# Kernel tuning notes

Measured on AMD Instinct MI355X. Metric: run time of the kernel, lower is better.

## Reference

```python
import jax, jax.numpy as jnp
import numpy as np

EMBED = 256
B, S = 4, 4096

def _linear_params(key, d):
    k1, k2 = jax.random.split(key)
    lim = 1.0 / np.sqrt(d)
    W = jax.random.uniform(k1, (d, d), jnp.float32, -lim, lim)
    b = jax.random.uniform(k2, (d,), jnp.float32, -lim, lim)
    return W, b

def setup_inputs() -> dict:
    key = jax.random.key(0)
    ks = jax.random.split(key, 6)
    x = jax.random.normal(ks[0], (B, S, EMBED), jnp.float32)
    Wq, bq = _linear_params(ks[1], EMBED)
    Wk, bk = _linear_params(ks[2], EMBED)
    Wv, bv = _linear_params(ks[3], EMBED)
    Wl, bl = _linear_params(ks[4], EMBED)
    g1 = jnp.ones((EMBED,), jnp.float32); be1 = jnp.zeros((EMBED,), jnp.float32)
    g2 = jnp.ones((EMBED,), jnp.float32); be2 = jnp.zeros((EMBED,), jnp.float32)
    return {"x": x, "Wq": Wq, "bq": bq, "Wk": Wk, "bk": bk, "Wv": Wv, "bv": bv,
            "Wl": Wl, "bl": bl, "g1": g1, "be1": be1, "g2": g2, "be2": be2}

def _layernorm(x, g, b, eps=1e-5):
    mu = jnp.mean(x, axis=-1, keepdims=True)
    var = jnp.mean(jnp.square(x - mu), axis=-1, keepdims=True)
    return (x - mu) * jax.lax.rsqrt(var + eps) * g + b

def reference(x, Wq, bq, Wk, bk, Wv, bv, Wl, bl, g1, be1, g2, be2):
    d = x.shape[-1]
    q = jnp.einsum('bsd,ed->bse', x, Wq) + bq
    k = jnp.einsum('bsd,ed->bse', x, Wk) + bk
    v = jnp.einsum('bsd,ed->bse', x, Wv) + bv
    scores = jnp.einsum('bqd,bkd->bqk', q, k) / np.sqrt(d).astype(np.float32)
    attn = jax.nn.softmax(scores, axis=-1)
    out = jnp.einsum('bqk,bkd->bqd', attn, v)
    h = _layernorm(x + out, g1, be1)
    # NOTE: same linear applied twice (as in the original module)
    h = jnp.einsum('bsd,ed->bse', h, Wl) + bl
    h = jax.nn.relu(h)
    h = jnp.einsum('bsd,ed->bse', h, Wl) + bl
    return _layernorm(x + h, g2, be2)
```

## Files before the change

### kernel.cpp

```cpp
#include <hip/hip_runtime.h>

typedef unsigned short u16;
typedef float  f32x4 __attribute__((ext_vector_type(4)));
typedef short  s16x8 __attribute__((ext_vector_type(8)));
typedef unsigned short u16x4 __attribute__((ext_vector_type(4)));

__device__ __forceinline__ u16 f2b(float f) {
    unsigned b = __float_as_uint(f);
    return (u16)((b + 0x7FFFu + ((b >> 16) & 1u)) >> 16);
}
__device__ __forceinline__ float b2f(u16 u) { return __uint_as_float(((unsigned)u) << 16); }

__device__ __forceinline__ int perm64(int r) {
    return (r & 0x23) | (((r >> 2) & 3) << 3) | (((r >> 4) & 1) << 2);
}

__global__ __launch_bounds__(256) void cvt_f2b_k(const float* __restrict__ src, u16* __restrict__ dst, int n) {
    int i = (blockIdx.x * 256 + threadIdx.x) * 4;
    if (i < n) {
        f32x4 v = *(const f32x4*)(src + i);
        u16x4 o;
        o[0] = f2b(v[0]); o[1] = f2b(v[1]); o[2] = f2b(v[2]); o[3] = f2b(v[3]);
        *(u16x4*)(dst + i) = o;
    }
}

template<int TRANS, int RELU>
__global__ __launch_bounds__(256) void gemm_k256(const u16* __restrict__ A, const u16* __restrict__ W,
                                                 const float* __restrict__ bias, u16* __restrict__ Cd,
                                                 float scale) {
    const int tid = threadIdx.x;
    const int wv = tid >> 6, lane = tid & 63, g = lane >> 4, lq = lane & 15;
    const int m0 = blockIdx.x * 64, n0 = blockIdx.y * 64;

    const u16* arow = A + (size_t)(m0 + wv * 16 + lq) * 256;
    f32x4 acc[4];
#pragma unroll
    for (int nf = 0; nf < 4; ++nf) { acc[nf][0] = 0.f; acc[nf][1] = 0.f; acc[nf][2] = 0.f; acc[nf][3] = 0.f; }

#pragma unroll
    for (int kk = 0; kk < 8; ++kk) {
        s16x8 a = *(const s16x8*)(arow + kk * 32 + g * 8);
#pragma unroll
        for (int nf = 0; nf < 4; ++nf) {
            s16x8 b = *(const s16x8*)(W + (size_t)(n0 + nf * 16 + lq) * 256 + kk * 32 + g * 8);
            acc[nf] = __builtin_amdgcn_mfma_f32_16x16x32_bf16(a, b, acc[nf], 0, 0, 0);
        }
    }

    __shared__ __align__(16) u16 c_lds[64 * 64];
#pragma unroll
    for (int nf = 0; nf < 4; ++nf) {
        float bb = bias[n0 + nf * 16 + lq];
#pragma unroll
        for (int j = 0; j < 4; ++j) {
            float v = acc[nf][j] + bb;
            if (RELU) v = fmaxf(v, 0.f);
            v *= scale;
            if (!TRANS) c_lds[(wv * 16 + (g << 2) + j) * 64 + nf * 16 + lq] = f2b(v);
            else        c_lds[(nf * 16 + lq) * 64 + wv * 16 + (g << 2) + j] = f2b(v);
        }
    }
    __syncthreads();
    if (!TRANS) {
#pragma unroll
        for (int r = 0; r < 2; ++r) {
            int o = (r * 256 + tid) * 8, row = o >> 6, col = o & 63;
            *(s16x8*)(Cd + (size_t)(m0 + row) * 256 + n0 + col) = *(const s16x8*)(c_lds + row * 64 + col);
        }
    } else {
        int bidx = m0 >> 12, s0 = m0 & 4095;
#pragma unroll
        for (int r = 0; r < 2; ++r) {
            int o = (r * 256 + tid) * 8, drow = o >> 6, col = o & 63;
            *(s16x8*)(Cd + (size_t)bidx * 256 * 4096 + (size_t)(n0 + drow) * 4096 + s0 + col) =
                *(const s16x8*)(c_lds + drow * 64 + col);
        }
    }
}

__global__ __launch_bounds__(256) void flash_attn(const u16* __restrict__ Q, const u16* __restrict__ K,
                                                  const u16* __restrict__ VT, u16* __restrict__ O) {
    __shared__ __align__(16) u16 smem[32768];
    u16* k_lds = smem;
    u16* v_lds = smem + 16384;

    const int tid = threadIdx.x;
    const int wv = tid >> 6, lane = tid & 63, g = lane >> 4, lq = lane & 15;
    const int bqt = blockIdx.x, b = bqt >> 6, q0 = (bqt & 63) << 6;

    const u16* qrow = Q + (size_t)(b * 4096 + q0 + wv * 16 + lq) * 256;
    s16x8 qf[8];
#pragma unroll
    for (int kk = 0; kk < 8; ++kk) qf[kk] = *(const s16x8*)(qrow + kk * 32 + g * 8);

    f32x4 acc[16];
#pragma unroll
    for (int nf = 0; nf < 16; ++nf) { acc[nf][0] = 0.f; acc[nf][1] = 0.f; acc[nf][2] = 0.f; acc[nf][3] = 0.f; }
    float m_run = -3.0e38f, l_run = 0.f;

    const u16* kbase = K + (size_t)b * 4096 * 256;
    const u16* vbase = VT + (size_t)b * 256 * 4096;

    for (int t = 0; t < 64; ++t) {
        const int kv0 = t * 64;
#pragma unroll
        for (int r = 0; r < 8; ++r) {
            int o16 = r * 256 + tid;
            int row = o16 >> 5, c16 = o16 & 31;
            int prow = perm64(row);
            s16x8 val = *(const s16x8*)(kbase + (size_t)(kv0 + prow) * 256 + c16 * 8);
            *(s16x8*)(k_lds + ((row << 5) + (c16 ^ (row & 7))) * 8) = val;
        }
#pragma unroll
        for (int r = 0; r < 8; ++r) {
            int o16 = r * 256 + tid;
            int row = o16 >> 3, c16 = o16 & 7;
            s16x8 val = *(const s16x8*)(vbase + (size_t)row * 4096 + kv0 + c16 * 8);
            *(s16x8*)(v_lds + ((row << 3) + (c16 ^ (row & 7))) * 8) = val;
        }
        __syncthreads();

        f32x4 st[4];
#pragma unroll
        for (int f = 0; f < 4; ++f) { st[f][0] = 0.f; st[f][1] = 0.f; st[f][2] = 0.f; st[f][3] = 0.f; }
#pragma unroll
        for (int kk = 0; kk < 8; ++kk) {
#pragma unroll
            for (int f = 0; f < 4; ++f) {
                int row = f * 16 + lq;
                s16x8 a = *(const s16x8*)(k_lds + ((row << 5) + (((kk << 2) + g) ^ (row & 7))) * 8);
                st[f] = __builtin_amdgcn_mfma_f32_16x16x32_bf16(a, qf[kk], st[f], 0, 0, 0);
            }
        }

        float rm = -3.0e38f;
#pragma unroll
        for (int f = 0; f < 4; ++f)
            rm = fmaxf(rm, fmaxf(fmaxf(st[f][0], st[f][1]), fmaxf(st[f][2], st[f][3])));
        rm = fmaxf(rm, __shfl_xor(rm, 16));
        rm = fmaxf(rm, __shfl_xor(rm, 32));
        float mnew = fmaxf(m_run, rm);
        float alpha = __expf(m_run - mnew);
        float p[4][4]; float ps = 0.f;
#pragma unroll
        for (int f = 0; f < 4; ++f)
#pragma unroll
            for (int j = 0; j < 4; ++j) { float e = __expf(st[f][j] - mnew); p[f][j] = e; ps += e; }
        ps += __shfl_xor(ps, 16);
        ps += __shfl_xor(ps, 32);
        l_run = l_run * alpha + ps;
        m_run = mnew;
#pragma unroll
        for (int j = 0; j < 4; ++j) {
            float a4 = __shfl(alpha, (g << 2) + j);
#pragma unroll
            for (int nf = 0; nf < 16; ++nf) acc[nf][j] *= a4;
        }
        s16x8 pa[2];
#pragma unroll
        for (int kk = 0; kk < 2; ++kk) {
            union { s16x8 v; u16 u[8]; } pu;
#pragma unroll
            for (int j2 = 0; j2 < 4; ++j2) { pu.u[j2] = f2b(p[2 * kk][j2]); pu.u[4 + j2] = f2b(p[2 * kk + 1][j2]); }
            pa[kk] = pu.v;
        }
#pragma unroll
        for (int kk = 0; kk < 2; ++kk) {
#pragma unroll
            for (int nf = 0; nf < 16; ++nf) {
                int row = (nf << 4) + lq;
                s16x8 bv = *(const s16x8*)(v_lds + ((row << 3) + (((kk << 2) + g) ^ (row & 7))) * 8);
                acc[nf] = __builtin_amdgcn_mfma_f32_16x16x32_bf16(pa[kk], bv, acc[nf], 0, 0, 0);
            }
        }
        __syncthreads();
    }

    float linv[4];
#pragma unroll
    for (int j = 0; j < 4; ++j) linv[j] = 1.0f / __shfl(l_run, (g << 2) + j);
    float* o_lds = (float*)smem;
#pragma unroll
    for (int nf = 0; nf < 16; ++nf)
#pragma unroll
        for (int j = 0; j < 4; ++j)
            o_lds[(wv * 16 + (g << 2) + j) * 256 + (nf << 4) + lq] = acc[nf][j] * linv[j];
    __syncthreads();
    u16* orow = O + (size_t)(b * 4096 + q0) * 256;
#pragma unroll
    for (int r = 0; r < 8; ++r) {
        int o = (r * 256 + tid) * 8, row = o >> 8, col = o & 255;
        const float* src = o_lds + row * 256 + col;
        union { s16x8 v; u16 u[8]; } pu;
#pragma unroll
        for (int e = 0; e < 8; ++e) pu.u[e] = f2b(src[e]);
        *(s16x8*)(orow + (size_t)row * 256 + col) = pu.v;
    }
}

template<int OUTF32>
__global__ __launch_bounds__(256) void ln_k(const float* __restrict__ x, const u16* __restrict__ add,
                                            const float* __restrict__ gam, const float* __restrict__ bet,
                                            float* __restrict__ outf, u16* __restrict__ outb) {
    const int row = blockIdx.x * 4 + (threadIdx.x >> 6);
    const int lane = threadIdx.x & 63;
    f32x4 xv = *(const f32x4*)(x + (size_t)row * 256 + lane * 4);
    u16x4 av = *(const u16x4*)(add + (size_t)row * 256 + lane * 4);
    float s[4];
#pragma unroll
    for (int i = 0; i < 4; ++i) s[i] = xv[i] + b2f(av[i]);
    float sum = s[0] + s[1] + s[2] + s[3];
    float sq = s[0] * s[0] + s[1] * s[1] + s[2] * s[2] + s[3] * s[3];
#pragma unroll
    for (int d = 1; d < 64; d <<= 1) { sum += __shfl_xor(sum, d); sq += __shfl_xor(sq, d); }
    float mean = sum * (1.f / 256.f);
    float var = sq * (1.f / 256.f) - mean * mean;
    float rstd = rsqrtf(var + 1e-5f);
    f32x4 gv = *(const f32x4*)(gam + lane * 4);
    f32x4 bv = *(const f32x4*)(bet + lane * 4);
    if (OUTF32) {
        f32x4 y;
#pragma unroll
        for (int i = 0; i < 4; ++i) y[i] = (s[i] - mean) * rstd * gv[i] + bv[i];
        *(f32x4*)(outf + (size_t)row * 256 + lane * 4) = y;
    } else {
        u16x4 y;
#pragma unroll
        for (int i = 0; i < 4; ++i) y[i] = f2b((s[i] - mean) * rstd * gv[i] + bv[i]);
        *(u16x4*)(outb + (size_t)row * 256 + lane * 4) = y;
    }
}

extern "C" void kernel_launch(void* const* d_in, const int* in_sizes, int n_in,
                              void* d_out, int out_size, void* d_ws, size_t ws_size,
                              hipStream_t stream) {
    const float* x   = (const float*)d_in[0];
    const float* Wq  = (const float*)d_in[1];
    const float* bq  = (const float*)d_in[2];
    const float* Wk  = (const float*)d_in[3];
    const float* bk  = (const float*)d_in[4];
    const float* Wv  = (const float*)d_in[5];
    const float* bv  = (const float*)d_in[6];
    const float* Wl  = (const float*)d_in[7];
    const float* bl  = (const float*)d_in[8];
    const float* g1  = (const float*)d_in[9];
    const float* be1 = (const float*)d_in[10];
    const float* g2  = (const float*)d_in[11];
    const float* be2 = (const float*)d_in[12];
    float* out = (float*)d_out;

    const size_t NT = 16384 * 256;
    u16* xb  = (u16*)d_ws;
    u16* qb  = xb  + NT;
    u16* kb  = qb  + NT;
    u16* vtb = kb  + NT;
    u16* wqb = vtb + NT;
    u16* wkb = wqb + 65536;
    u16* wvb = wkb + 65536;
    u16* wlb = wvb + 65536;

    cvt_f2b_k<<<4096, 256, 0, stream>>>(x, xb, 4194304);
    cvt_f2b_k<<<64, 256, 0, stream>>>(Wq, wqb, 65536);
    cvt_f2b_k<<<64, 256, 0, stream>>>(Wk, wkb, 65536);
    cvt_f2b_k<<<64, 256, 0, stream>>>(Wv, wvb, 65536);
    cvt_f2b_k<<<64, 256, 0, stream>>>(Wl, wlb, 65536);

    dim3 ggrid(256, 4);
    gemm_k256<0, 0><<<ggrid, 256, 0, stream>>>(xb, wqb, bq, qb, 0.0625f);
    gemm_k256<0, 0><<<ggrid, 256, 0, stream>>>(xb, wkb, bk, kb, 1.0f);
    gemm_k256<1, 0><<<ggrid, 256, 0, stream>>>(xb, wvb, bv, vtb, 1.0f);

    flash_attn<<<256, 256, 0, stream>>>(qb, kb, vtb, xb );

    ln_k<0><<<4096, 256, 0, stream>>>(x, xb, g1, be1, nullptr, qb );

    gemm_k256<0, 1><<<ggrid, 256, 0, stream>>>(qb, wlb, bl, kb , 1.0f);
    gemm_k256<0, 0><<<ggrid, 256, 0, stream>>>(kb, wlb, bl, vtb , 1.0f);

    ln_k<1><<<4096, 256, 0, stream>>>(x, vtb, g2, be2, out, nullptr);
}
```

Measured before the change: 384.7 us.

## Rewrite flash attention with split-KV, async LDS double buffering, and lazy rescale

Replaces the attention kernel with a version where each block processes 128 queries (two 16-row groups per wave, sharing each K/V fragment). The KV range is split in two across a grid dimension, and a recombine kernel merges the partial outputs. K/V tiles are brought in with global_load_lds into a double-buffered LDS ring so loads overlap compute. Softmax uses exp2 with log2e folded into the Q scale, and the accumulator rescale is skipped when the running max grows by at most 8. The costs are extra partial-output memory traffic, a second kernel launch, and bf16 rounding of the partial outputs before combining.

```diff
diff --git a/kernel.cpp b/kernel.cpp
--- a/kernel.cpp
+++ b/kernel.cpp
@@ -13,6 +13,13 @@
 
 __device__ __forceinline__ int perm64(int r) {
     return (r & 0x23) | (((r >> 2) & 3) << 3) | (((r >> 4) & 1) << 2);
+}
+
+__device__ __forceinline__ void gload16(const u16* g, u16* l) {
+    __builtin_amdgcn_global_load_lds(
+        (const __attribute__((address_space(1))) unsigned int*)g,
+        (__attribute__((address_space(3))) unsigned int*)l,
+        16, 0, 0);
 }
 
 __global__ __launch_bounds__(256) void cvt_f2b_k(const float* __restrict__ src, u16* __restrict__ dst, int n) {
@@ -79,124 +86,178 @@
     }
 }
 
-__global__ __launch_bounds__(256) void flash_attn(const u16* __restrict__ Q, const u16* __restrict__ K,
-                                                  const u16* __restrict__ VT, u16* __restrict__ O) {
-    __shared__ __align__(16) u16 smem[32768];
-    u16* k_lds = smem;
-    u16* v_lds = smem + 16384;
-
+__global__ __launch_bounds__(256, 1) void flash2(const u16* __restrict__ Q, const u16* __restrict__ K,
+                                                 const u16* __restrict__ VT, u16* __restrict__ Opart,
+                                                 float* __restrict__ ml) {
+    __shared__ __align__(16) u16 smem[65536];
     const int tid = threadIdx.x;
-    const int wv = tid >> 6, lane = tid & 63, g = lane >> 4, lq = lane & 15;
-    const int bqt = blockIdx.x, b = bqt >> 6, q0 = (bqt & 63) << 6;
-
-    const u16* qrow = Q + (size_t)(b * 4096 + q0 + wv * 16 + lq) * 256;
-    s16x8 qf[8];
-#pragma unroll
-    for (int kk = 0; kk < 8; ++kk) qf[kk] = *(const s16x8*)(qrow + kk * 32 + g * 8);
-
-    f32x4 acc[16];
-#pragma unroll
-    for (int nf = 0; nf < 16; ++nf) { acc[nf][0] = 0.f; acc[nf][1] = 0.f; acc[nf][2] = 0.f; acc[nf][3] = 0.f; }
-    float m_run = -3.0e38f, l_run = 0.f;
-
-    const u16* kbase = K + (size_t)b * 4096 * 256;
-    const u16* vbase = VT + (size_t)b * 256 * 4096;
-
-    for (int t = 0; t < 64; ++t) {
-        const int kv0 = t * 64;
-#pragma unroll
-        for (int r = 0; r < 8; ++r) {
-            int o16 = r * 256 + tid;
-            int row = o16 >> 5, c16 = o16 & 31;
-            int prow = perm64(row);
-            s16x8 val = *(const s16x8*)(kbase + (size_t)(kv0 + prow) * 256 + c16 * 8);
-            *(s16x8*)(k_lds + ((row << 5) + (c16 ^ (row & 7))) * 8) = val;
-        }
-#pragma unroll
-        for (int r = 0; r < 8; ++r) {
-            int o16 = r * 256 + tid;
-            int row = o16 >> 3, c16 = o16 & 7;
-            s16x8 val = *(const s16x8*)(vbase + (size_t)row * 4096 + kv0 + c16 * 8);
-            *(s16x8*)(v_lds + ((row << 3) + (c16 ^ (row & 7))) * 8) = val;
-        }
+    const int wv = tid >> 6, lane = tid & 63, g = lane >> 4, lqi = lane & 15;
+    const int bx = blockIdx.x, s = blockIdx.y;
+    const int b = bx >> 5, q0 = (bx & 31) << 7;
+    const int kvbase = s * 2048;
+
+    const u16* kb_ = K + (size_t)b * 4096 * 256;
+    const u16* vb_ = VT + (size_t)b * 256 * 4096;
+
+    s16x8 qf[2][8];
+#pragma unroll
+    for (int qh = 0; qh < 2; ++qh) {
+        const u16* qrow = Q + (size_t)(b * 4096 + q0 + wv * 32 + qh * 16 + lqi) * 256;
+#pragma unroll
+        for (int kk = 0; kk < 8; ++kk) qf[qh][kk] = *(const s16x8*)(qrow + kk * 32 + g * 8);
+    }
+
+    int koff[8], voff[8];
+#pragma unroll
+    for (int r = 0; r < 8; ++r) {
+        int row = r * 8 + (tid >> 5), ch = tid & 31;
+        koff[r] = perm64(row) * 256 + ((ch ^ (row & 7)) << 3);
+        int vrow = r * 32 + (tid >> 3), vch = tid & 7;
+        voff[r] = vrow * 4096 + ((vch ^ (vrow & 7)) << 3);
+    }
+
+    f32x4 acc[2][16];
+#pragma unroll
+    for (int qh = 0; qh < 2; ++qh)
+#pragma unroll
+        for (int nf = 0; nf < 16; ++nf) { acc[qh][nf][0]=0.f; acc[qh][nf][1]=0.f; acc[qh][nf][2]=0.f; acc[qh][nf][3]=0.f; }
+    float mrun[2] = {-1e30f, -1e30f}, lrun[2] = {0.f, 0.f};
+
+    auto STAGE = [&](int bufsel, int t) {
+        const u16* kt = kb_ + (size_t)(kvbase + (t << 6)) * 256;
+        const u16* vt = vb_ + (kvbase + (t << 6));
+        u16* kl = smem + bufsel * 32768 + tid * 8;
+        u16* vl = kl + 16384;
+#pragma unroll
+        for (int r = 0; r < 8; ++r) gload16(kt + koff[r], kl + r * 2048);
+#pragma unroll
+        for (int r = 0; r < 8; ++r) gload16(vt + voff[r], vl + r * 2048);
+    };
+
+    auto COMPUTE = [&](int bufsel) {
+        const u16* kbuf = smem + bufsel * 32768;
+        const u16* vbuf = kbuf + 16384;
+        f32x4 st[2][4];
+#pragma unroll
+        for (int qh = 0; qh < 2; ++qh)
+#pragma unroll
+            for (int f = 0; f < 4; ++f) { st[qh][f][0]=0.f; st[qh][f][1]=0.f; st[qh][f][2]=0.f; st[qh][f][3]=0.f; }
+#pragma unroll
+        for (int kk = 0; kk < 8; ++kk) {
+#pragma unroll
+            for (int f = 0; f < 4; ++f) {
+                int row = f * 16 + lqi;
+                s16x8 a = *(const s16x8*)(kbuf + ((row << 5) + (((kk << 2) + g) ^ (row & 7))) * 8);
+                st[0][f] = __builtin_amdgcn_mfma_f32_16x16x32_bf16(a, qf[0][kk], st[0][f], 0, 0, 0);
+                st[1][f] = __builtin_amdgcn_mfma_f32_16x16x32_bf16(a, qf[1][kk], st[1][f], 0, 0, 0);
+            }
+        }
+        s16x8 pa[2][2];
+#pragma unroll
+        for (int qh = 0; qh < 2; ++qh) {
+            float rm = -1e30f;
+#pragma unroll
+            for (int f = 0; f < 4; ++f)
+                rm = fmaxf(rm, fmaxf(fmaxf(st[qh][f][0], st[qh][f][1]), fmaxf(st[qh][f][2], st[qh][f][3])));
+            rm = fmaxf(rm, __shfl_xor(rm, 16));
+            rm = fmaxf(rm, __shfl_xor(rm, 32));
+            if (!__all(rm - mrun[qh] <= 8.f)) {
+                float mnew = fmaxf(mrun[qh], rm);
+                float alpha = exp2f(mrun[qh] - mnew);
+#pragma unroll
+                for (int j = 0; j < 4; ++j) {
+                    float a4 = __shfl(alpha, (g << 2) + j);
+#pragma unroll
+                    for (int nf = 0; nf < 16; ++nf) acc[qh][nf][j] *= a4;
+                }
+                mrun[qh] = mnew;
+                lrun[qh] *= alpha;
+            }
+            float ps = 0.f;
+#pragma unroll
+            for (int f = 0; f < 4; ++f)
+#pragma unroll
+                for (int j = 0; j < 4; ++j) { float e = exp2f(st[qh][f][j] - mrun[qh]); st[qh][f][j] = e; ps += e; }
+            ps += __shfl_xor(ps, 16);
+            ps += __shfl_xor(ps, 32);
+            lrun[qh] += ps;
+#pragma unroll
+            for (int kk2 = 0; kk2 < 2; ++kk2) {
+                union { s16x8 v; u16 u[8]; } pu;
+#pragma unroll
+                for (int j2 = 0; j2 < 4; ++j2) { pu.u[j2] = f2b(st[qh][2*kk2][j2]); pu.u[4+j2] = f2b(st[qh][2*kk2+1][j2]); }
+                pa[qh][kk2] = pu.v;
+            }
+        }
+#pragma unroll
+        for (int kk2 = 0; kk2 < 2; ++kk2) {
+#pragma unroll
+            for (int nf = 0; nf < 16; ++nf) {
+                int row = (nf << 4) + lqi;
+                s16x8 bv = *(const s16x8*)(vbuf + ((row << 3) + (((kk2 << 2) + g) ^ (row & 7))) * 8);
+                acc[0][nf] = __builtin_amdgcn_mfma_f32_16x16x32_bf16(pa[0][kk2], bv, acc[0][nf], 0, 0, 0);
+                acc[1][nf] = __builtin_amdgcn_mfma_f32_16x16x32_bf16(pa[1][kk2], bv, acc[1][nf], 0, 0, 0);
+            }
+        }
+    };
+
+    STAGE(0, 0);
+    for (int t2 = 0; t2 < 32; t2 += 2) {
         __syncthreads();
-
-        f32x4 st[4];
-#pragma unroll
-        for (int f = 0; f < 4; ++f) { st[f][0] = 0.f; st[f][1] = 0.f; st[f][2] = 0.f; st[f][3] = 0.f; }
-#pragma unroll
-        for (int kk = 0; kk < 8; ++kk) {
-#pragma unroll
-            for (int f = 0; f < 4; ++f) {
-                int row = f * 16 + lq;
-                s16x8 a = *(const s16x8*)(k_lds + ((row << 5) + (((kk << 2) + g) ^ (row & 7))) * 8);
-                st[f] = __builtin_amdgcn_mfma_f32_16x16x32_bf16(a, qf[kk], st[f], 0, 0, 0);
-            }
-        }
-
-        float rm = -3.0e38f;
-#pragma unroll
-        for (int f = 0; f < 4; ++f)
-            rm = fmaxf(rm, fmaxf(fmaxf(st[f][0], st[f][1]), fmaxf(st[f][2], st[f][3])));
-        rm = fmaxf(rm, __shfl_xor(rm, 16));
-        rm = fmaxf(rm, __shfl_xor(rm, 32));
-        float mnew = fmaxf(m_run, rm);
-        float alpha = __expf(m_run - mnew);
-        float p[4][4]; float ps = 0.f;
-#pragma unroll
-        for (int f = 0; f < 4; ++f)
-#pragma unroll
-            for (int j = 0; j < 4; ++j) { float e = __expf(st[f][j] - mnew); p[f][j] = e; ps += e; }
-        ps += __shfl_xor(ps, 16);
-        ps += __shfl_xor(ps, 32);
-        l_run = l_run * alpha + ps;
-        m_run = mnew;
-#pragma unroll
-        for (int j = 0; j < 4; ++j) {
-            float a4 = __shfl(alpha, (g << 2) + j);
-#pragma unroll
-            for (int nf = 0; nf < 16; ++nf) acc[nf][j] *= a4;
-        }
-        s16x8 pa[2];
-#pragma unroll
-        for (int kk = 0; kk < 2; ++kk) {
-            union { s16x8 v; u16 u[8]; } pu;
-#pragma unroll
-            for (int j2 = 0; j2 < 4; ++j2) { pu.u[j2] = f2b(p[2 * kk][j2]); pu.u[4 + j2] = f2b(p[2 * kk + 1][j2]); }
-            pa[kk] = pu.v;
-        }
-#pragma unroll
-        for (int kk = 0; kk < 2; ++kk) {
-#pragma unroll
-            for (int nf = 0; nf < 16; ++nf) {
-                int row = (nf << 4) + lq;
-                s16x8 bv = *(const s16x8*)(v_lds + ((row << 3) + (((kk << 2) + g) ^ (row & 7))) * 8);
-                acc[nf] = __builtin_amdgcn_mfma_f32_16x16x32_bf16(pa[kk], bv, acc[nf], 0, 0, 0);
-            }
-        }
+        STAGE(1, t2 + 1);
+        COMPUTE(0);
         __syncthreads();
-    }
-
-    float linv[4];
-#pragma unroll
-    for (int j = 0; j < 4; ++j) linv[j] = 1.0f / __shfl(l_run, (g << 2) + j);
-    float* o_lds = (float*)smem;
-#pragma unroll
-    for (int nf = 0; nf < 16; ++nf)
-#pragma unroll
-        for (int j = 0; j < 4; ++j)
-            o_lds[(wv * 16 + (g << 2) + j) * 256 + (nf << 4) + lq] = acc[nf][j] * linv[j];
+        if (t2 + 2 < 32) STAGE(0, t2 + 2);
+        COMPUTE(1);
+    }
+
     __syncthreads();
-    u16* orow = O + (size_t)(b * 4096 + q0) * 256;
-#pragma unroll
-    for (int r = 0; r < 8; ++r) {
+    float linv[2][4];
+#pragma unroll
+    for (int qh = 0; qh < 2; ++qh)
+#pragma unroll
+        for (int j = 0; j < 4; ++j) linv[qh][j] = 1.0f / __shfl(lrun[qh], (g << 2) + j);
+    u16* o_lds = smem;
+#pragma unroll
+    for (int qh = 0; qh < 2; ++qh)
+#pragma unroll
+        for (int nf = 0; nf < 16; ++nf)
+#pragma unroll
+            for (int j = 0; j < 4; ++j)
+                o_lds[(wv * 32 + qh * 16 + (g << 2) + j) * 256 + (nf << 4) + lqi] = f2b(acc[qh][nf][j] * linv[qh][j]);
+    __syncthreads();
+    u16* orow = Opart + (size_t)s * 4194304 + (size_t)(b * 4096 + q0) * 256;
+#pragma unroll
+    for (int r = 0; r < 16; ++r) {
         int o = (r * 256 + tid) * 8, row = o >> 8, col = o & 255;
-        const float* src = o_lds + row * 256 + col;
-        union { s16x8 v; u16 u[8]; } pu;
-#pragma unroll
-        for (int e = 0; e < 8; ++e) pu.u[e] = f2b(src[e]);
-        *(s16x8*)(orow + (size_t)row * 256 + col) = pu.v;
-    }
+        *(s16x8*)(orow + (size_t)row * 256 + col) = *(const s16x8*)(o_lds + row * 256 + col);
+    }
+    if (lane < 16) {
+#pragma unroll
+        for (int qh = 0; qh < 2; ++qh) {
+            int grow = b * 4096 + q0 + wv * 32 + qh * 16 + lqi;
+            ml[s * 32768 + grow]         = mrun[qh];
+            ml[s * 32768 + 16384 + grow] = lrun[qh];
+        }
+    }
+}
+
+__global__ __launch_bounds__(256) void recomb_k(const u16* __restrict__ Opart, const float* __restrict__ ml,
+                                                u16* __restrict__ out) {
+    const int row = blockIdx.x * 4 + (threadIdx.x >> 6);
+    const int lane = threadIdx.x & 63;
+    float m0 = ml[row],          l0 = ml[16384 + row];
+    float m1 = ml[32768 + row],  l1 = ml[49152 + row];
+    float mm = fmaxf(m0, m1);
+    float a0 = l0 * exp2f(m0 - mm), a1 = l1 * exp2f(m1 - mm);
+    float rs = 1.0f / (a0 + a1);
+    a0 *= rs; a1 *= rs;
+    u16x4 v0 = *(const u16x4*)(Opart + (size_t)row * 256 + lane * 4);
+    u16x4 v1 = *(const u16x4*)(Opart + 4194304 + (size_t)row * 256 + lane * 4);
+    u16x4 o;
+#pragma unroll
+    for (int i = 0; i < 4; ++i) o[i] = f2b(a0 * b2f(v0[i]) + a1 * b2f(v1[i]));
+    *(u16x4*)(out + (size_t)row * 256 + lane * 4) = o;
 }
 
 template<int OUTF32>
@@ -255,10 +316,12 @@
     u16* qb  = xb  + NT;
     u16* kb  = qb  + NT;
     u16* vtb = kb  + NT;
-    u16* wqb = vtb + NT;
+    u16* o01 = vtb + NT;
+    u16* wqb = o01 + 2 * NT;
     u16* wkb = wqb + 65536;
     u16* wvb = wkb + 65536;
     u16* wlb = wvb + 65536;
+    float* ml = (float*)(wlb + 65536);
 
     cvt_f2b_k<<<4096, 256, 0, stream>>>(x, xb, 4194304);
     cvt_f2b_k<<<64, 256, 0, stream>>>(Wq, wqb, 65536);
@@ -267,11 +330,12 @@
     cvt_f2b_k<<<64, 256, 0, stream>>>(Wl, wlb, 65536);
 
     dim3 ggrid(256, 4);
-    gemm_k256<0, 0><<<ggrid, 256, 0, stream>>>(xb, wqb, bq, qb, 0.0625f);
+    gemm_k256<0, 0><<<ggrid, 256, 0, stream>>>(xb, wqb, bq, qb, 0.0625f * 1.44269504f);
     gemm_k256<0, 0><<<ggrid, 256, 0, stream>>>(xb, wkb, bk, kb, 1.0f);
     gemm_k256<1, 0><<<ggrid, 256, 0, stream>>>(xb, wvb, bv, vtb, 1.0f);
 
-    flash_attn<<<256, 256, 0, stream>>>(qb, kb, vtb, xb );
+    flash2<<<dim3(128, 2), 256, 0, stream>>>(qb, kb, vtb, o01, ml);
+    recomb_k<<<4096, 256, 0, stream>>>(o01, ml, xb );
 
     ln_k<0><<<4096, 256, 0, stream>>>(x, xb, g1, be1, nullptr, qb );
 
```

Result: faster. 371.1 us (-3.5%).
